# Kernel tuning notes

Measured on AMD Instinct MI355X. Metric: run time of the kernel, lower is better.

Reference implementation:

```python
import jax, jax.numpy as jnp
import numpy as np

N_NODES = 100000


def gcn_conv(x, W, b, src, dst, n):
    # PyG GCNConv: h = X @ W, add self-loops, symmetric normalization, scatter-add, + bias
    h = x @ W  # [N, out]
    loop = jnp.arange(n, dtype=src.dtype)
    src2 = jnp.concatenate([src, loop])
    dst2 = jnp.concatenate([dst, loop])
    ew = jnp.ones(src2.shape[0], dtype=h.dtype)
    deg = jax.ops.segment_sum(ew, dst2, num_segments=n)  # in-degree incl. self-loop
    dinv = jnp.where(deg > 0, jax.lax.rsqrt(deg), 0.0)
    norm = dinv[src2] * dinv[dst2]  # [E+N]
    msg = h[src2] * norm[:, None]  # gather + scale
    out = jax.ops.segment_sum(msg, dst2, num_segments=n)  # scatter-add
    return out + b


def setup_inputs() -> dict:
    key = jax.random.key(0)
    k1, k2, k3, k4, k5 = jax.random.split(key, 5)
    n, e = N_NODES, 3200000
    d_in, d_hid, d_out = 512, 16, 7
    x = jax.random.normal(k1, (n, d_in), dtype=jnp.float32)
    edge_index = jax.random.randint(k2, (2, e), 0, n, dtype=jnp.int64)
    W1 = jax.random.normal(k3, (d_in, d_hid), dtype=jnp.float32) / np.sqrt(d_in)
    b1 = jnp.zeros((d_hid,), dtype=jnp.float32)
    W2 = jax.random.normal(k4, (d_hid, d_out), dtype=jnp.float32) / np.sqrt(d_hid)
    b2 = jnp.zeros((d_out,), dtype=jnp.float32)
    return {"x": x, "edge_index": edge_index, "W1": W1, "b1": b1, "W2": W2, "b2": b2}


def reference(x, edge_index, W1, b1, W2, b2):
    n = x.shape[0]
    src, dst = edge_index[0], edge_index[1]
    h = jax.nn.relu(gcn_conv(x, W1, b1, src, dst, n))
    # dropout is identity in eval mode
    h = gcn_conv(h, W2, b2, src, dst, n)
    return jax.nn.log_softmax(h, axis=1)
```

## Files before the change

### kernel.cpp

```cpp
#include <hip/hip_runtime.h>
#include <math.h>

#define D_IN 512
#define F1   16
#define F2   7

#define BKT_SHIFT 8
#define PK_SHIFT  18
#define PK_MASK   ((1u << PK_SHIFT) - 1u)
#define A_CHUNK   8192
#define B_CAP     16384

typedef float vf4 __attribute__((ext_vector_type(4)));

__global__ __launch_bounds__(256) void binhist_kernel(const int* __restrict__ dst,
                                                      int* __restrict__ bucket_cnt,
                                                      int E, int NB) {
    __shared__ int lh[512];
    for (int i = threadIdx.x; i < 512; i += 256) lh[i] = 0;
    __syncthreads();
    int base = blockIdx.x * A_CHUNK;
#pragma unroll
    for (int i = 0; i < A_CHUNK / 256; ++i) {
        int t = base + i * 256 + threadIdx.x;
        if (t < E) {
            int d = __builtin_nontemporal_load(&dst[t]);
            atomicAdd(&lh[d >> BKT_SHIFT], 1);
        }
    }
    __syncthreads();
    for (int i = threadIdx.x; i < NB; i += 256) {
        int v = lh[i];
        if (v) atomicAdd(&bucket_cnt[i], v);
    }
}

__global__ __launch_bounds__(512) void bucketscan_kernel(const int* __restrict__ bucket_cnt,
                                                         int* __restrict__ bucket_base,
                                                         int* __restrict__ bucket_cursor,
                                                         int NB, int E) {
    __shared__ int sm[512];
    int tid = threadIdx.x;
    int v = (tid < NB) ? bucket_cnt[tid] : 0;
    sm[tid] = v;
    __syncthreads();
    for (int off = 1; off < 512; off <<= 1) {
        int t = (tid >= off) ? sm[tid - off] : 0;
        __syncthreads();
        sm[tid] += t;
        __syncthreads();
    }
    if (tid < NB) {
        int ex = sm[tid] - v;
        bucket_base[tid] = ex;
        bucket_cursor[tid] = ex;
    }
    if (tid == 0) bucket_base[NB] = E;
}

__global__ __launch_bounds__(256) void bin_kernel(const int* __restrict__ src,
                                                  const int* __restrict__ dst,
                                                  int* __restrict__ bucket_cursor,
                                                  unsigned int* __restrict__ binned,
                                                  int E, int NB) {
    __shared__ int lh[512];
    __shared__ int lbase[512];
    __shared__ int lcur[512];
    __shared__ int sdelta[512];
    __shared__ int sA[512], sB[512];
    __shared__ unsigned int rbuf[A_CHUNK];
    __shared__ int rdelta[A_CHUNK];
    int tid = threadIdx.x;
    for (int i = tid; i < 512; i += 256) lh[i] = 0;
    __syncthreads();

    int base = blockIdx.x * A_CHUNK;
    int dcache[A_CHUNK / 256];
    int scache[A_CHUNK / 256];
#pragma unroll
    for (int i = 0; i < A_CHUNK / 256; ++i) {
        int t = base + i * 256 + tid;
        int d = -1, s = 0;
        if (t < E) {
            d = __builtin_nontemporal_load(&dst[t]);
            s = __builtin_nontemporal_load(&src[t]);
            atomicAdd(&lh[d >> BKT_SHIFT], 1);
        }
        dcache[i] = d;
        scache[i] = s;
    }
    __syncthreads();

    for (int i = tid; i < 512; i += 256) sA[i] = lh[i];
    __syncthreads();
    int* psrc = sA; int* pdst = sB;
    for (int off = 1; off < 512; off <<= 1) {
        for (int i = tid; i < 512; i += 256)
            pdst[i] = psrc[i] + ((i >= off) ? psrc[i - off] : 0);
        __syncthreads();
        int* tmp = psrc; psrc = pdst; pdst = tmp;
    }
    for (int i = tid; i < 512; i += 256) {
        int ex = psrc[i] - lh[i];
        lbase[i] = ex;
        lcur[i] = ex;
    }
    __syncthreads();

    for (int b = tid; b < NB; b += 256) {
        int c = lh[b];
        int g = c ? atomicAdd(&bucket_cursor[b], c) : 0;
        sdelta[b] = g - lbase[b];
    }
    __syncthreads();

#pragma unroll
    for (int i = 0; i < A_CHUNK / 256; ++i) {
        int d = dcache[i];
        if (d >= 0) {
            int b = d >> BKT_SHIFT;
            int p = atomicAdd(&lcur[b], 1);
            rbuf[p] = (unsigned int)scache[i] | ((unsigned int)(d & 255) << PK_SHIFT);
            rdelta[p] = sdelta[b];
        }
    }
    __syncthreads();

    int total = min(A_CHUNK, E - base);
    for (int p = tid; p < total; p += 256)
        binned[rdelta[p] + p] = rbuf[p];
}

__global__ __launch_bounds__(256) void csr_kernel(const unsigned int* __restrict__ binned,
                                                  const int* __restrict__ bucket_base,
                                                  int* __restrict__ row_ptr,
                                                  int* __restrict__ row_end,
                                                  float* __restrict__ dinv,
                                                  int* __restrict__ adj, int n) {
    __shared__ int lh[256], lscan[256], lcur[256];
    __shared__ unsigned int rbuf[B_CAP];
    int b = blockIdx.x;
    int tid = threadIdx.x;
    int gbase = bucket_base[b];
    int gend  = bucket_base[b + 1];
    int m = gend - gbase;
    lh[tid] = 0;
    __syncthreads();
    for (int i = tid; i < m; i += 256) {
        unsigned int w = __builtin_nontemporal_load(&binned[gbase + i]);
        if (i < B_CAP) rbuf[i] = w;
        atomicAdd(&lh[w >> PK_SHIFT], 1);
    }
    __syncthreads();
    int v = lh[tid];
    lscan[tid] = v;
    __syncthreads();
    for (int off = 1; off < 256; off <<= 1) {
        int t = (tid >= off) ? lscan[tid - off] : 0;
        __syncthreads();
        lscan[tid] += t;
        __syncthreads();
    }
    int ex = lscan[tid] - v;
    int node = (b << BKT_SHIFT) + tid;
    if (node < n) {
        row_ptr[node] = gbase + ex;
        row_end[node] = gbase + ex + v;
        dinv[node] = rsqrtf((float)v + 1.0f);
    }
    lcur[tid] = ex;
    __syncthreads();
    for (int i = tid; i < m; i += 256) {
        unsigned int w = (i < B_CAP) ? rbuf[i] : binned[gbase + i];
        int d = (int)(w >> PK_SHIFT);
        int s = (int)(w & PK_MASK);
        int p = atomicAdd(&lcur[d], 1);
        adj[gbase + p] = s;
    }
}

__global__ __launch_bounds__(256, 2) void mm1_kernel(const float* __restrict__ x,
                                                     const float* __restrict__ W1,
                                                     const float* __restrict__ dinv,
                                                     float* __restrict__ h1s, int n) {
    int tid = threadIdx.x;
    int lane = tid & 63;
    int wid  = blockIdx.x * 4 + (tid >> 6);
    int nwaves = gridDim.x * 4;

    float wA[4][16], wB[4][16];
#pragma unroll
    for (int r = 0; r < 4; ++r) {
        const float4* ra = (const float4*)(W1 + (size_t)(4 * lane + r) * F1);
        const float4* rb = (const float4*)(W1 + (size_t)(256 + 4 * lane + r) * F1);
#pragma unroll
        for (int q = 0; q < 4; ++q) {
            float4 va = ra[q], vb = rb[q];
            wA[r][4 * q + 0] = va.x; wA[r][4 * q + 1] = va.y;
            wA[r][4 * q + 2] = va.z; wA[r][4 * q + 3] = va.w;
            wB[r][4 * q + 0] = vb.x; wB[r][4 * q + 1] = vb.y;
            wB[r][4 * q + 2] = vb.z; wB[r][4 * q + 3] = vb.w;
        }
    }

    int node = wid;
    if (node >= n) return;
    const float* xb = x + (size_t)node * D_IN;
    vf4 pA = *(const vf4*)(xb + 4 * lane);
    vf4 pB = *(const vf4*)(xb + 256 + 4 * lane);

    while (node < n) {
        vf4 xA = pA, xB = pB;
        int nx = node + nwaves;
        if (nx < n) {
            const float* xn = x + (size_t)nx * D_IN;
            pA = *(const vf4*)(xn + 4 * lane);
            pB = *(const vf4*)(xn + 256 + 4 * lane);
        }
        float acc[16];
#pragma unroll
        for (int f = 0; f < 16; ++f) acc[f] = 0.f;
#pragma unroll
        for (int r = 0; r < 4; ++r) {
            float ea = xA[r], eb = xB[r];
#pragma unroll
            for (int f = 0; f < 16; ++f) {
                acc[f] += ea * wA[r][f];
                acc[f] += eb * wB[r][f];
            }
        }
        int h0 = lane & 1, h1 = lane & 2, h2 = lane & 4, h3 = lane & 8;
        float a[8];
#pragma unroll
        for (int j = 0; j < 8; ++j) {
            float keep = h0 ? acc[2 * j + 1] : acc[2 * j];
            float give = h0 ? acc[2 * j] : acc[2 * j + 1];
            a[j] = keep + __shfl_xor(give, 1);
        }
        float b[4];
#pragma unroll
        for (int j = 0; j < 4; ++j) {
            float keep = h1 ? a[2 * j + 1] : a[2 * j];
            float give = h1 ? a[2 * j] : a[2 * j + 1];
            b[j] = keep + __shfl_xor(give, 2);
        }
        float c[2];
#pragma unroll
        for (int j = 0; j < 2; ++j) {
            float keep = h2 ? b[2 * j + 1] : b[2 * j];
            float give = h2 ? b[2 * j] : b[2 * j + 1];
            c[j] = keep + __shfl_xor(give, 4);
        }
        float d = (h3 ? c[1] : c[0]) + __shfl_xor(h3 ? c[0] : c[1], 8);
        d += __shfl_xor(d, 16);
        d += __shfl_xor(d, 32);
        if (lane < 16) {
            float di = dinv[node];
            h1s[(size_t)node * F1 + lane] = d * di;
        }
        node = nx;
    }
}

__global__ __launch_bounds__(256) void agg1_kernel(const int* __restrict__ row_ptr,
                                                   const int* __restrict__ row_end,
                                                   const int* __restrict__ adj,
                                                   const float* __restrict__ h,
                                                   const float* __restrict__ dinv,
                                                   const float* __restrict__ b1,
                                                   const float* __restrict__ W2,
                                                   float* __restrict__ h2s, int n) {
    int t = blockIdx.x * 256 + threadIdx.x;
    int node = t >> 4;
    if (node >= n) return;
    int li = t & 15;
    int jq = li & 3;
    int e4 = li >> 2;
    int s = row_ptr[node], e = row_end[node];
    vf4 a0 = {0.f, 0.f, 0.f, 0.f}, a1 = {0.f, 0.f, 0.f, 0.f};
    int k = s + e4;
    for (; k + 4 < e; k += 8) {
        int s0 = adj[k], s1 = adj[k + 4];
        a0 += *(const vf4*)(h + (size_t)s0 * F1 + jq * 4);
        a1 += *(const vf4*)(h + (size_t)s1 * F1 + jq * 4);
    }
    if (k < e) a0 += *(const vf4*)(h + (size_t)adj[k] * F1 + jq * 4);
    vf4 sum = a0 + a1;
#pragma unroll
    for (int q = 0; q < 4; ++q) {
        sum[q] += __shfl_xor(sum[q], 4, 16);
        sum[q] += __shfl_xor(sum[q], 8, 16);
    }
    float di = dinv[node];
    vf4 self = *(const vf4*)(h + (size_t)node * F1 + jq * 4);
    float v0 = di * (sum[0] + self[0]) + b1[jq * 4 + 0]; v0 = v0 > 0.f ? v0 : 0.f;
    float v1 = di * (sum[1] + self[1]) + b1[jq * 4 + 1]; v1 = v1 > 0.f ? v1 : 0.f;
    float v2 = di * (sum[2] + self[2]) + b1[jq * 4 + 2]; v2 = v2 > 0.f ? v2 : 0.f;
    float v3 = di * (sum[3] + self[3]) + b1[jq * 4 + 3]; v3 = v3 > 0.f ? v3 : 0.f;
    const float* w0 = W2 + (size_t)(jq * 4 + 0) * F2;
    const float* w1 = W2 + (size_t)(jq * 4 + 1) * F2;
    const float* w2 = W2 + (size_t)(jq * 4 + 2) * F2;
    const float* w3 = W2 + (size_t)(jq * 4 + 3) * F2;
    float p0 = v0 * w0[0] + v1 * w1[0] + v2 * w2[0] + v3 * w3[0];
    float p1 = v0 * w0[1] + v1 * w1[1] + v2 * w2[1] + v3 * w3[1];
    float p2 = v0 * w0[2] + v1 * w1[2] + v2 * w2[2] + v3 * w3[2];
    float p3 = v0 * w0[3] + v1 * w1[3] + v2 * w2[3] + v3 * w3[3];
    float p4 = v0 * w0[4] + v1 * w1[4] + v2 * w2[4] + v3 * w3[4];
    float p5 = v0 * w0[5] + v1 * w1[5] + v2 * w2[5] + v3 * w3[5];
    float p6 = v0 * w0[6] + v1 * w1[6] + v2 * w2[6] + v3 * w3[6];
    p0 += __shfl_xor(p0, 1, 16); p0 += __shfl_xor(p0, 2, 16);
    p1 += __shfl_xor(p1, 1, 16); p1 += __shfl_xor(p1, 2, 16);
    p2 += __shfl_xor(p2, 1, 16); p2 += __shfl_xor(p2, 2, 16);
    p3 += __shfl_xor(p3, 1, 16); p3 += __shfl_xor(p3, 2, 16);
    p4 += __shfl_xor(p4, 1, 16); p4 += __shfl_xor(p4, 2, 16);
    p5 += __shfl_xor(p5, 1, 16); p5 += __shfl_xor(p5, 2, 16);
    p6 += __shfl_xor(p6, 1, 16); p6 += __shfl_xor(p6, 2, 16);
    if (li < 8) {
        float oc = li == 0 ? p0 : li == 1 ? p1 : li == 2 ? p2 : li == 3 ? p3
                 : li == 4 ? p4 : li == 5 ? p5 : li == 6 ? p6 : 0.0f;
        h2s[(size_t)node * 8 + li] = oc * di;
    }
}

__global__ __launch_bounds__(256) void agg2_kernel(const int* __restrict__ row_ptr,
                                                   const int* __restrict__ row_end,
                                                   const int* __restrict__ adj,
                                                   const float* __restrict__ h,
                                                   const float* __restrict__ dinv,
                                                   const float* __restrict__ b2,
                                                   float* __restrict__ out, int n) {
    int t = blockIdx.x * 256 + threadIdx.x;
    int node = t >> 3;
    if (node >= n) return;
    int li = t & 7;
    int jh = li & 1;
    int e4 = li >> 1;
    int s = row_ptr[node], e = row_end[node];
    vf4 a0 = {0.f, 0.f, 0.f, 0.f}, a1 = {0.f, 0.f, 0.f, 0.f};
    int k = s + e4;
    for (; k + 4 < e; k += 8) {
        int s0 = adj[k], s1 = adj[k + 4];
        a0 += *(const vf4*)(h + (size_t)s0 * 8 + jh * 4);
        a1 += *(const vf4*)(h + (size_t)s1 * 8 + jh * 4);
    }
    if (k < e) a0 += *(const vf4*)(h + (size_t)adj[k] * 8 + jh * 4);
    vf4 sum = a0 + a1;
#pragma unroll
    for (int q = 0; q < 4; ++q) {
        sum[q] += __shfl_xor(sum[q], 2, 8);
        sum[q] += __shfl_xor(sum[q], 4, 8);
    }
    float di = dinv[node];
    vf4 self = *(const vf4*)(h + (size_t)node * 8 + jh * 4);
    float v0 = di * (sum[0] + self[0]) + (jh ? b2[4] : b2[0]);
    float v1 = di * (sum[1] + self[1]) + (jh ? b2[5] : b2[1]);
    float v2 = di * (sum[2] + self[2]) + (jh ? b2[6] : b2[2]);
    float v3 = jh ? -INFINITY : di * (sum[3] + self[3]) + b2[3];
    float m4 = fmaxf(fmaxf(v0, v1), fmaxf(v2, v3));
    float m = fmaxf(m4, __shfl_xor(m4, 1, 8));
    float es = expf(v0 - m) + expf(v1 - m) + expf(v2 - m) + (jh ? 0.f : expf(v3 - m));
    float ssum = es + __shfl_xor(es, 1, 8);
    float lse = m + logf(ssum);
    float* op = out + (size_t)node * F2 + jh * 4;
    op[0] = v0 - lse; op[1] = v1 - lse; op[2] = v2 - lse;
    if (!jh) op[3] = v3 - lse;
}

extern "C" void kernel_launch(void* const* d_in, const int* in_sizes, int n_in,
                              void* d_out, int out_size, void* d_ws, size_t ws_size,
                              hipStream_t stream) {
    const float* x  = (const float*)d_in[0];
    const int*   ei = (const int*)d_in[1];
    const float* W1 = (const float*)d_in[2];
    const float* b1 = (const float*)d_in[3];
    const float* W2 = (const float*)d_in[4];
    const float* b2 = (const float*)d_in[5];

    int n = in_sizes[0] / D_IN;
    int E = in_sizes[1] / 2;
    const int* src = ei;
    const int* dst = ei + E;
    int NB = (n + 255) >> BKT_SHIFT;

    char* ws = (char*)d_ws;
    size_t o = 0;
    int* bucket_cnt    = (int*)(ws + o); o += 512 * 4;
    int* bucket_base   = (int*)(ws + o); o += 516 * 4;
    int* bucket_cursor = (int*)(ws + o); o += 512 * 4;
    int*   row_ptr = (int*)(ws + o);   o += (size_t)n * 4;
    int*   row_end = (int*)(ws + o);   o += (size_t)n * 4;
    float* dinv    = (float*)(ws + o); o += (size_t)n * 4;
    int*   adj     = (int*)(ws + o);   o += (size_t)E * 4;
    size_t uni = (size_t)E > (size_t)n * 32 ? (size_t)E : (size_t)n * 32;
    unsigned int* binned = (unsigned int*)(ws + o);
    float* h1s = (float*)(ws + o);
    float* h2s = (float*)(ws + o) + (size_t)n * F1;
    o += uni * 4;
    float* out = (float*)d_out;

    const int B = 256;
    int GA = (E + A_CHUNK - 1) / A_CHUNK;

    hipMemsetAsync(bucket_cnt, 0, 512 * sizeof(int), stream);

    binhist_kernel<<<GA, B, 0, stream>>>(dst, bucket_cnt, E, NB);
    bucketscan_kernel<<<1, 512, 0, stream>>>(bucket_cnt, bucket_base, bucket_cursor, NB, E);
    bin_kernel<<<GA, B, 0, stream>>>(src, dst, bucket_cursor, binned, E, NB);
    csr_kernel<<<NB, B, 0, stream>>>(binned, bucket_base, row_ptr, row_end, dinv, adj, n);

    mm1_kernel<<<512, B, 0, stream>>>(x, W1, dinv, h1s, n);

    agg1_kernel<<<((size_t)n * F1 + B - 1) / B, B, 0, stream>>>(row_ptr, row_end, adj, h1s, dinv, b1, W2, h2s, n);

    agg2_kernel<<<((size_t)n * 8 + B - 1) / B, B, 0, stream>>>(row_ptr, row_end, adj, h2s, dinv, b2, out, n);
}
```

Baseline: 471.2 us.

## Build CSR with global degree atomics and scatter instead of bucket sort

Replaces the two-pass bucketed binning and per-bucket local CSR construction with a simpler pipeline. It counts in-degree with global atomics, scans hierarchically to get row pointers, then scatters edges using per-node atomic cursors. This removes the intermediate binned buffer and the shared-memory sorting work. In exchange, it issues many random global atomics and scattered writes to adj, and row order becomes nondeterministic.

```diff
diff --git a/kernel.cpp b/kernel.cpp
--- a/kernel.cpp
+++ b/kernel.cpp
@@ -5,177 +5,95 @@
 #define F1   16
 #define F2   7
 
-#define BKT_SHIFT 8
-#define PK_SHIFT  18
-#define PK_MASK   ((1u << PK_SHIFT) - 1u)
-#define A_CHUNK   8192
-#define B_CAP     16384
-
 typedef float vf4 __attribute__((ext_vector_type(4)));
-
-__global__ __launch_bounds__(256) void binhist_kernel(const int* __restrict__ dst,
-                                                      int* __restrict__ bucket_cnt,
-                                                      int E, int NB) {
-    __shared__ int lh[512];
-    for (int i = threadIdx.x; i < 512; i += 256) lh[i] = 0;
+typedef int   vi4 __attribute__((ext_vector_type(4)));
+
+__global__ __launch_bounds__(256) void deg_kernel(const int* __restrict__ dst,
+                                                  int* __restrict__ deg, int E) {
+    int i = (blockIdx.x * 256 + threadIdx.x) * 4;
+    if (i + 4 <= E) {
+        vi4 d = __builtin_nontemporal_load((const vi4*)(dst + i));
+        atomicAdd(&deg[d[0]], 1);
+        atomicAdd(&deg[d[1]], 1);
+        atomicAdd(&deg[d[2]], 1);
+        atomicAdd(&deg[d[3]], 1);
+    } else {
+        for (; i < E; ++i) atomicAdd(&deg[dst[i]], 1);
+    }
+}
+
+__global__ __launch_bounds__(512) void degsum_kernel(const int* __restrict__ deg,
+                                                     int* __restrict__ bsum, int n) {
+    __shared__ int sm[512];
+    int t = threadIdx.x;
+    int i = blockIdx.x * 512 + t;
+    sm[t] = i < n ? deg[i] : 0;
     __syncthreads();
-    int base = blockIdx.x * A_CHUNK;
-#pragma unroll
-    for (int i = 0; i < A_CHUNK / 256; ++i) {
-        int t = base + i * 256 + threadIdx.x;
-        if (t < E) {
-            int d = __builtin_nontemporal_load(&dst[t]);
-            atomicAdd(&lh[d >> BKT_SHIFT], 1);
-        }
-    }
+    for (int off = 256; off; off >>= 1) {
+        if (t < off) sm[t] += sm[t + off];
+        __syncthreads();
+    }
+    if (t == 0) bsum[blockIdx.x] = sm[0];
+}
+
+__global__ __launch_bounds__(256) void bscan_kernel(int* __restrict__ bsum, int NBLK) {
+    __shared__ int sm[256];
+    int t = threadIdx.x;
+    int v = t < NBLK ? bsum[t] : 0;
+    sm[t] = v;
     __syncthreads();
-    for (int i = threadIdx.x; i < NB; i += 256) {
-        int v = lh[i];
-        if (v) atomicAdd(&bucket_cnt[i], v);
-    }
-}
-
-__global__ __launch_bounds__(512) void bucketscan_kernel(const int* __restrict__ bucket_cnt,
-                                                         int* __restrict__ bucket_base,
-                                                         int* __restrict__ bucket_cursor,
-                                                         int NB, int E) {
+    for (int off = 1; off < 256; off <<= 1) {
+        int u = (t >= off) ? sm[t - off] : 0;
+        __syncthreads();
+        sm[t] += u;
+        __syncthreads();
+    }
+    if (t < NBLK) bsum[t] = sm[t] - v;
+}
+
+__global__ __launch_bounds__(512) void rowptr_kernel(int* __restrict__ deg_cursor,
+                                                     const int* __restrict__ bsum,
+                                                     int* __restrict__ row_ptr,
+                                                     int* __restrict__ row_end,
+                                                     float* __restrict__ dinv, int n) {
     __shared__ int sm[512];
-    int tid = threadIdx.x;
-    int v = (tid < NB) ? bucket_cnt[tid] : 0;
-    sm[tid] = v;
+    int t = threadIdx.x;
+    int i = blockIdx.x * 512 + t;
+    int d = i < n ? deg_cursor[i] : 0;
+    sm[t] = d;
     __syncthreads();
     for (int off = 1; off < 512; off <<= 1) {
-        int t = (tid >= off) ? sm[tid - off] : 0;
-        __syncthreads();
-        sm[tid] += t;
-        __syncthreads();
-    }
-    if (tid < NB) {
-        int ex = sm[tid] - v;
-        bucket_base[tid] = ex;
-        bucket_cursor[tid] = ex;
-    }
-    if (tid == 0) bucket_base[NB] = E;
-}
-
-__global__ __launch_bounds__(256) void bin_kernel(const int* __restrict__ src,
-                                                  const int* __restrict__ dst,
-                                                  int* __restrict__ bucket_cursor,
-                                                  unsigned int* __restrict__ binned,
-                                                  int E, int NB) {
-    __shared__ int lh[512];
-    __shared__ int lbase[512];
-    __shared__ int lcur[512];
-    __shared__ int sdelta[512];
-    __shared__ int sA[512], sB[512];
-    __shared__ unsigned int rbuf[A_CHUNK];
-    __shared__ int rdelta[A_CHUNK];
-    int tid = threadIdx.x;
-    for (int i = tid; i < 512; i += 256) lh[i] = 0;
-    __syncthreads();
-
-    int base = blockIdx.x * A_CHUNK;
-    int dcache[A_CHUNK / 256];
-    int scache[A_CHUNK / 256];
-#pragma unroll
-    for (int i = 0; i < A_CHUNK / 256; ++i) {
-        int t = base + i * 256 + tid;
-        int d = -1, s = 0;
-        if (t < E) {
-            d = __builtin_nontemporal_load(&dst[t]);
-            s = __builtin_nontemporal_load(&src[t]);
-            atomicAdd(&lh[d >> BKT_SHIFT], 1);
-        }
-        dcache[i] = d;
-        scache[i] = s;
-    }
-    __syncthreads();
-
-    for (int i = tid; i < 512; i += 256) sA[i] = lh[i];
-    __syncthreads();
-    int* psrc = sA; int* pdst = sB;
-    for (int off = 1; off < 512; off <<= 1) {
-        for (int i = tid; i < 512; i += 256)
-            pdst[i] = psrc[i] + ((i >= off) ? psrc[i - off] : 0);
-        __syncthreads();
-        int* tmp = psrc; psrc = pdst; pdst = tmp;
-    }
-    for (int i = tid; i < 512; i += 256) {
-        int ex = psrc[i] - lh[i];
-        lbase[i] = ex;
-        lcur[i] = ex;
-    }
-    __syncthreads();
-
-    for (int b = tid; b < NB; b += 256) {
-        int c = lh[b];
-        int g = c ? atomicAdd(&bucket_cursor[b], c) : 0;
-        sdelta[b] = g - lbase[b];
-    }
-    __syncthreads();
-
-#pragma unroll
-    for (int i = 0; i < A_CHUNK / 256; ++i) {
-        int d = dcache[i];
-        if (d >= 0) {
-            int b = d >> BKT_SHIFT;
-            int p = atomicAdd(&lcur[b], 1);
-            rbuf[p] = (unsigned int)scache[i] | ((unsigned int)(d & 255) << PK_SHIFT);
-            rdelta[p] = sdelta[b];
-        }
-    }
-    __syncthreads();
-
-    int total = min(A_CHUNK, E - base);
-    for (int p = tid; p < total; p += 256)
-        binned[rdelta[p] + p] = rbuf[p];
-}
-
-__global__ __launch_bounds__(256) void csr_kernel(const unsigned int* __restrict__ binned,
-                                                  const int* __restrict__ bucket_base,
-                                                  int* __restrict__ row_ptr,
-                                                  int* __restrict__ row_end,
-                                                  float* __restrict__ dinv,
-                                                  int* __restrict__ adj, int n) {
-    __shared__ int lh[256], lscan[256], lcur[256];
-    __shared__ unsigned int rbuf[B_CAP];
-    int b = blockIdx.x;
-    int tid = threadIdx.x;
-    int gbase = bucket_base[b];
-    int gend  = bucket_base[b + 1];
-    int m = gend - gbase;
-    lh[tid] = 0;
-    __syncthreads();
-    for (int i = tid; i < m; i += 256) {
-        unsigned int w = __builtin_nontemporal_load(&binned[gbase + i]);
-        if (i < B_CAP) rbuf[i] = w;
-        atomicAdd(&lh[w >> PK_SHIFT], 1);
-    }
-    __syncthreads();
-    int v = lh[tid];
-    lscan[tid] = v;
-    __syncthreads();
-    for (int off = 1; off < 256; off <<= 1) {
-        int t = (tid >= off) ? lscan[tid - off] : 0;
-        __syncthreads();
-        lscan[tid] += t;
-        __syncthreads();
-    }
-    int ex = lscan[tid] - v;
-    int node = (b << BKT_SHIFT) + tid;
-    if (node < n) {
-        row_ptr[node] = gbase + ex;
-        row_end[node] = gbase + ex + v;
-        dinv[node] = rsqrtf((float)v + 1.0f);
-    }
-    lcur[tid] = ex;
-    __syncthreads();
-    for (int i = tid; i < m; i += 256) {
-        unsigned int w = (i < B_CAP) ? rbuf[i] : binned[gbase + i];
-        int d = (int)(w >> PK_SHIFT);
-        int s = (int)(w & PK_MASK);
-        int p = atomicAdd(&lcur[d], 1);
-        adj[gbase + p] = s;
+        int u = (t >= off) ? sm[t - off] : 0;
+        __syncthreads();
+        sm[t] += u;
+        __syncthreads();
+    }
+    if (i < n) {
+        int ex = sm[t] - d + bsum[blockIdx.x];
+        row_ptr[i] = ex;
+        row_end[i] = ex + d;
+        dinv[i] = rsqrtf((float)d + 1.0f);
+        deg_cursor[i] = ex;
+    }
+}
+
+__global__ __launch_bounds__(256) void scatter_kernel(const int* __restrict__ src,
+                                                      const int* __restrict__ dst,
+                                                      int* __restrict__ cursor,
+                                                      int* __restrict__ adj, int E) {
+    int i = (blockIdx.x * 256 + threadIdx.x) * 4;
+    if (i + 4 <= E) {
+        vi4 s = __builtin_nontemporal_load((const vi4*)(src + i));
+        vi4 d = __builtin_nontemporal_load((const vi4*)(dst + i));
+        int p0 = atomicAdd(&cursor[d[0]], 1); adj[p0] = s[0];
+        int p1 = atomicAdd(&cursor[d[1]], 1); adj[p1] = s[1];
+        int p2 = atomicAdd(&cursor[d[2]], 1); adj[p2] = s[2];
+        int p3 = atomicAdd(&cursor[d[3]], 1); adj[p3] = s[3];
+    } else {
+        for (; i < E; ++i) {
+            int p = atomicAdd(&cursor[dst[i]], 1);
+            adj[p] = src[i];
+        }
     }
 }
 
@@ -380,33 +298,30 @@
     int E = in_sizes[1] / 2;
     const int* src = ei;
     const int* dst = ei + E;
-    int NB = (n + 255) >> BKT_SHIFT;
+    int NBLK = (n + 511) >> 9;
 
     char* ws = (char*)d_ws;
     size_t o = 0;
-    int* bucket_cnt    = (int*)(ws + o); o += 512 * 4;
-    int* bucket_base   = (int*)(ws + o); o += 516 * 4;
-    int* bucket_cursor = (int*)(ws + o); o += 512 * 4;
     int*   row_ptr = (int*)(ws + o);   o += (size_t)n * 4;
     int*   row_end = (int*)(ws + o);   o += (size_t)n * 4;
     float* dinv    = (float*)(ws + o); o += (size_t)n * 4;
+    int*   cursor  = (int*)(ws + o);   o += (size_t)n * 4;
+    int*   bsum    = (int*)(ws + o);   o += 256 * 4;
     int*   adj     = (int*)(ws + o);   o += (size_t)E * 4;
-    size_t uni = (size_t)E > (size_t)n * 32 ? (size_t)E : (size_t)n * 32;
-    unsigned int* binned = (unsigned int*)(ws + o);
-    float* h1s = (float*)(ws + o);
-    float* h2s = (float*)(ws + o) + (size_t)n * F1;
-    o += uni * 4;
+    float* h1s     = (float*)(ws + o); o += (size_t)n * F1 * 4;
+    float* h2s     = (float*)(ws + o); o += (size_t)n * 8 * 4;
     float* out = (float*)d_out;
 
     const int B = 256;
-    int GA = (E + A_CHUNK - 1) / A_CHUNK;
-
-    hipMemsetAsync(bucket_cnt, 0, 512 * sizeof(int), stream);
-
-    binhist_kernel<<<GA, B, 0, stream>>>(dst, bucket_cnt, E, NB);
-    bucketscan_kernel<<<1, 512, 0, stream>>>(bucket_cnt, bucket_base, bucket_cursor, NB, E);
-    bin_kernel<<<GA, B, 0, stream>>>(src, dst, bucket_cursor, binned, E, NB);
-    csr_kernel<<<NB, B, 0, stream>>>(binned, bucket_base, row_ptr, row_end, dinv, adj, n);
+    int GE = (E + 1023) / 1024;
+
+    hipMemsetAsync(cursor, 0, (size_t)n * sizeof(int), stream);
+
+    deg_kernel<<<GE, B, 0, stream>>>(dst, cursor, E);
+    degsum_kernel<<<NBLK, 512, 0, stream>>>(cursor, bsum, n);
+    bscan_kernel<<<1, 256, 0, stream>>>(bsum, NBLK);
+    rowptr_kernel<<<NBLK, 512, 0, stream>>>(cursor, bsum, row_ptr, row_end, dinv, n);
+    scatter_kernel<<<GE, B, 0, stream>>>(src, dst, cursor, adj, E);
 
     mm1_kernel<<<512, B, 0, stream>>>(x, W1, dinv, h1s, n);
 
```

Result: slower. 789.5 us (+67.6%).
